# Optimization experiments

Hardware: AMD Instinct MI355X
Metric: run time of the kernel (lower is better)

## Reference

```python
import jax, jax.numpy as jnp
from jax import lax
import numpy as np

S = 1024      # number of superpoints (all valid, 60 pts each >= min_points)
P = 60        # points per superpoint (labels are contiguous blocks)
K = 10        # sample_k FPS representatives
NM = 800      # total number of SAM masks
H = W = 256   # mask image dims
FD = 512      # point feature dim (clip_dim)
SAMPLE_K = 10
RADIUS = 0.2
MASK_THRES = 0.2
SIM_THRES = 0.5
N_MASK = 5
TOP_K = 10


def setup_inputs() -> dict:
    key = jax.random.key(0)
    ks = jax.random.split(key, 8)
    centers = jax.random.normal(ks[0], (S, 3), jnp.float32)
    # tight clusters around centers so the radius-0.2 graph has edges
    pcds = (centers[:, None, :] + 0.03 * jax.random.normal(ks[1], (S, P, 3), jnp.float32)).reshape(S * P, 3)
    spt_labels = jnp.repeat(jnp.arange(S, dtype=jnp.int32), P)
    masks = jax.random.bernoulli(ks[2], 0.05, (NM, H, W))
    y = jax.random.randint(ks[3], (S * P,), 0, H, jnp.int32)
    x = jax.random.randint(ks[4], (S * P,), 0, W, jnp.int32)
    vis = jax.random.bernoulli(ks[5], 0.7, (S * P,)).astype(jnp.int32)
    mapping = jnp.stack([jnp.zeros(S * P, jnp.int32), y, x, vis], axis=1)
    sam_scores = jax.random.uniform(ks[6], (NM,), jnp.float32, 0.5, 1.0)
    point_feas = jax.random.normal(ks[7], (S * P, FD), jnp.float32)
    return {"pcds": pcds, "spt_labels": spt_labels, "masks": masks,
            "mapping": mapping, "sam_scores": sam_scores, "point_feas": point_feas}


def _fps_idx(pts, k):
    # pts: [P,3]. Deterministic start at index 0 (torch version uses a random start).
    d0 = jnp.sum((pts - pts[0]) ** 2, axis=1)
    def step(dist, _):
        idx = jnp.argmax(dist)
        nd = jnp.sum((pts - pts[idx]) ** 2, axis=1)
        return jnp.minimum(dist, nd), idx
    _, rest = lax.scan(step, d0, None, length=k - 1)
    return jnp.concatenate([jnp.zeros((1,), rest.dtype), rest])


def _forward(pcds, sam_scores, point_feas, spt_labels, masks, mapping):
    N = pcds.shape[0]
    pts_g = pcds.reshape(S, P, 3)  # labels are contiguous blocks of size P
    idxs = jax.vmap(lambda p: _fps_idx(lax.stop_gradient(p), SAMPLE_K))(pts_g)      # [S,K]
    reps = jnp.take_along_axis(pts_g, idxs[:, :, None], axis=1)                     # [S,K,3]

    # pairwise min distance between superpoint representative sets
    flat = reps.reshape(S * K, 3)
    sq = jnp.sum(flat ** 2, axis=1)
    d2 = jnp.maximum(sq[:, None] + sq[None, :] - 2.0 * (flat @ flat.T), 0.0)
    d = jnp.sqrt(d2 + 1e-12)
    mind = d.reshape(S, K, S, K).min(axis=(1, 3))                                   # [S,S]
    eye = jnp.eye(S, dtype=bool)
    adj0 = jnp.where((mind < RADIUS) & ~eye, jnp.exp(-mind), 0.0)

    # mask coverage per point, aggregated per superpoint
    vis = mapping[:, 3] == 1
    yy = jnp.clip(mapping[:, 1], 0, H - 1)
    xx = jnp.clip(mapping[:, 2], 0, W - 1)
    coverage = (masks[:, yy, xx].T & vis[:, None]).astype(jnp.float32)              # [N,NM]
    counts = jax.ops.segment_sum(jnp.ones((N,), jnp.float32), spt_labels, num_segments=S)[:, None]
    cov_g = jax.ops.segment_sum(coverage, spt_labels, num_segments=S)               # [S,NM]
    frac = cov_g / (counts + 1e-6)

    # per-mask keep only top_k superpoints by coverage fraction
    _, tki = lax.top_k(frac.T, TOP_K)                                               # [NM,TOP_K]
    tkm = jnp.zeros((NM, S), bool).at[jnp.arange(NM)[:, None], tki].set(True).T      # [S,NM]
    frac = jnp.where(tkm, frac, 0.0)
    contrib = frac >= MASK_THRES                                                     # [S,NM] bool

    # mean point features per superpoint, L2-normalized
    feats = jax.ops.segment_sum(point_feas, spt_labels, num_segments=S) / (counts + 1e-6)
    feats = feats / jnp.maximum(jnp.linalg.norm(feats, axis=1, keepdims=True), 1e-12)

    def row_mod(i):
        mi = contrib[i]                                                              # [NM]
        union = (mi[None, :] | contrib).astype(jnp.float32)                          # [S,NM]
        _, tk = lax.top_k(union, N_MASK)                                             # [S,N_MASK]
        ti = jnp.take_along_axis(jnp.broadcast_to(mi[None, :], (S, NM)), tk, axis=1)
        tj = jnp.take_along_axis(contrib, tk, axis=1)
        inter = (ti & tj).sum(1).astype(jnp.float32)
        uni = (ti | tj).sum(1).astype(jnp.float32)
        ov = inter / (uni + 1e-6)
        sim = jnp.clip((feats @ feats[i] + 1.0) * 0.5, 0.0, 1.0)
        sim = jnp.where(sim < SIM_THRES, 1.0, sim)
        return ov * sim

    mod = lax.map(row_mod, jnp.arange(S))                                            # [S,S], symmetric
    adjacency = jnp.where(adj0 > 0, jnp.maximum(mod, adj0), 0.0)

    weights = frac * sam_scores[None, :]
    conf = jnp.clip(weights.sum(1) / (frac.sum(1) + 1e-6), 0.0, None)
    return adjacency, conf


def reference(pcds, spt_labels, masks, mapping, sam_scores, point_feas):
    return _forward(pcds, sam_scores, point_feas, spt_labels, masks, mapping)
```

## Files before the change

### kernel.cpp

```cpp
#include <hip/hip_runtime.h>
#include <hip/hip_bf16.h>

#define SNUM 1024
#define PNUM 60
#define KFPS 10
#define NMASK 800
#define WORDS 25
#define HWDIM 256
#define FD 512
#define NPTS (SNUM*PNUM)
#define EDGE_CAP (1u<<20)

__device__ __forceinline__ float fmul(float a, float b){ return __fmul_rn(a,b); }
__device__ __forceinline__ float fadd(float a, float b){ return __fadd_rn(a,b); }
__device__ __forceinline__ float fsub(float a, float b){ return __fsub_rn(a,b); }

__device__ __forceinline__ float dist2f(float ax,float ay,float az,float bx,float by,float bz){
    float dx=fsub(ax,bx), dy=fsub(ay,by), dz=fsub(az,bz);
    return fadd(fadd(fmul(dx,dx),fmul(dy,dy)),fmul(dz,dz));
}

__global__ __launch_bounds__(64) void k_initfps(const float* __restrict__ pcds,
                                                float* __restrict__ reps,
                                                unsigned int* __restrict__ zbase,
                                                const unsigned char* __restrict__ m8,
                                                unsigned int* __restrict__ dflag){
    int s = blockIdx.x;
    int l = threadIdx.x;
    if (s < 64){
        int tid = s*64 + l;
        #pragma unroll
        for (int k=0;k<8;++k){
            int wi = tid + k*4096;
            if (wi < 28673) zbase[wi] = 0u;
        }
        #pragma unroll
        for (int k=0;k<16;++k){
            int i = tid*16 + k;
            if ((i & 3) != 0 && m8[i] == 1){ atomicOr(dflag, 1u); break; }
        }
    }
    float x=0.f,y=0.f,z=0.f;
    if (l < PNUM){
        const float* p = pcds + (size_t)(s*PNUM + l)*3;
        x=p[0]; y=p[1]; z=p[2];
    }
    float x0=__shfl(x,0), y0=__shfl(y,0), z0=__shfl(z,0);
    float dist = dist2f(x,y,z,x0,y0,z0);
    int sel[KFPS];
    sel[0]=0;
    #pragma unroll
    for(int it=1; it<KFPS; ++it){
        float v = (l<PNUM)? dist : -INFINITY;
        int idx = l;
        #pragma unroll
        for(int off=32; off; off>>=1){
            float ov = __shfl_xor(v, off);
            int   oi = __shfl_xor(idx, off);
            if (ov > v || (ov==v && oi<idx)){ v=ov; idx=oi; }
        }
        sel[it]=idx;
        float sx=__shfl(x,idx), sy=__shfl(y,idx), sz=__shfl(z,idx);
        float nd = dist2f(x,y,z,sx,sy,sz);
        dist = fminf(dist, nd);
    }
    #pragma unroll
    for(int j=0;j<KFPS;++j){
        float rx=__shfl(x,sel[j]), ry=__shfl(y,sel[j]), rz=__shfl(z,sel[j]);
        if (l==0){
            float* o = reps + (size_t)(s*KFPS+j)*3;
            o[0]=rx; o[1]=ry; o[2]=rz;
        }
    }
}

__global__ __launch_bounds__(256) void k_pack(const unsigned char* __restrict__ m8,
                                              const int* __restrict__ m32,
                                              const unsigned int* __restrict__ flag,
                                              unsigned int* __restrict__ pb){
    __shared__ unsigned int lds[256*WORDS];
    int t = threadIdx.x;
    int wv = t >> 6, lane = t & 63;
    int pixBase = blockIdx.x * 256;
    if (*flag & 1u){
        const unsigned int* base32 = (const unsigned int*)m8;
        int pix4 = (pixBase >> 2) + lane;
        for (int w=wv; w<WORDS; w+=4){
            unsigned int w0=0,w1=0,w2=0,w3=0;
            #pragma unroll
            for (int b=0;b<32;++b){
                unsigned int u = base32[(size_t)(w*32+b)*16384 + pix4];
                w0 |= (u & 1u) << b;
                w1 |= ((u >> 8) & 1u) << b;
                w2 |= ((u >> 16) & 1u) << b;
                w3 |= ((u >> 24) & 1u) << b;
            }
            int p4 = lane*4;
            lds[(p4+0)*WORDS+w]=w0; lds[(p4+1)*WORDS+w]=w1;
            lds[(p4+2)*WORDS+w]=w2; lds[(p4+3)*WORDS+w]=w3;
        }
    } else {
        for (int w=wv; w<WORDS; w+=4){
            for (int i=0;i<4;++i){
                int pixel = pixBase + lane*4 + i;
                unsigned int word = 0;
                #pragma unroll
                for (int b=0;b<32;++b)
                    word |= (unsigned int)(m32[(size_t)(w*32+b)*65536 + pixel] & 1) << b;
                lds[(lane*4+i)*WORDS+w] = word;
            }
        }
    }
    __syncthreads();
    uint4* out4 = (uint4*)(pb + (size_t)pixBase*WORDS);
    const uint4* l4 = (const uint4*)lds;
    for (int u=t; u<1600; u+=256) out4[u] = l4[u];
}

__global__ __launch_bounds__(256) void k_cov(const int* __restrict__ mapping,
                                             const unsigned int* __restrict__ pb,
                                             unsigned char* __restrict__ cntT){
    __shared__ int pxl[8][PNUM];
    int t = threadIdx.x;
    int sBase = blockIdx.x * 8;
    for (int idx=t; idx<8*PNUM; idx+=256){
        int ls = idx / PNUM, p = idx - ls*PNUM;
        const int4 v = ((const int4*)mapping)[(sBase+ls)*PNUM + p];
        int y = min(max(v.y,0),HWDIM-1), x = min(max(v.z,0),HWDIM-1);
        pxl[ls][p] = (v.w==1) ? ((y<<8)|x) : -1;
    }
    __syncthreads();
    int ls = t >> 5, w = t & 31;
    if (w >= WORDS) return;
    unsigned int acc8[8];
    #pragma unroll
    for (int k=0;k<8;++k) acc8[k]=0;
    #pragma unroll 6
    for (int p=0;p<PNUM;++p){
        int px = pxl[ls][p];
        if (px >= 0){
            unsigned int word = pb[(size_t)px*WORDS + w];
            #pragma unroll
            for (int k=0;k<8;++k)
                acc8[k] += (word >> k) & 0x01010101u;
        }
    }
    int s = sBase + ls;
    #pragma unroll
    for (int k=0;k<8;++k)
        #pragma unroll
        for (int j=0;j<4;++j){
            int b = k + 8*j;
            cntT[(size_t)(w*32+b)*SNUM + s] = (unsigned char)((acc8[k] >> (8*j)) & 0xFF);
        }
}

__global__ __launch_bounds__(256) void k_topk(const unsigned char* __restrict__ cntT,
                                              const float* __restrict__ scores,
                                              unsigned int* __restrict__ contrib,
                                              float* __restrict__ wsum,
                                              float* __restrict__ fsum){
    int m = blockIdx.x;
    int t = threadIdx.x;
    __shared__ int hist[64];
    __shared__ int scan_s[256];
    __shared__ int sT, sR;
    if (t < 64) hist[t]=0;
    __syncthreads();
    uchar4 c4 = ((const uchar4*)(cntT + (size_t)m*SNUM))[t];
    int c[4] = {(int)c4.x,(int)c4.y,(int)c4.z,(int)c4.w};
    atomicAdd(&hist[c[0]],1); atomicAdd(&hist[c[1]],1);
    atomicAdd(&hist[c[2]],1); atomicAdd(&hist[c[3]],1);
    __syncthreads();
    if (t==0){
        int running=0, T=0, r=10;
        for(int v=63;v>=0;--v){
            int nr = running + hist[v];
            if (nr >= 10){ T=v; r=10-running; break; }
            running = nr;
        }
        sT=T; sR=r;
    }
    __syncthreads();
    int T=sT, r=sR;
    int eq = (c[0]==T)+(c[1]==T)+(c[2]==T)+(c[3]==T);
    scan_s[t]=eq; __syncthreads();
    for(int off=1;off<256;off<<=1){
        int v = (t>=off)? scan_s[t-off] : 0;
        __syncthreads();
        scan_s[t]+=v;
        __syncthreads();
    }
    int rank = scan_s[t]-eq;
    float sc = scores[m];
    #pragma unroll
    for(int j=0;j<4;++j){
        int s = t*4+j;
        bool selv = (c[j]>T) || (c[j]==T && rank<r);
        if (c[j]==T) rank++;
        if (selv && c[j]>0){
            float frac = (float)c[j]/60.0f;
            atomicAdd(&wsum[s], frac*sc);
            atomicAdd(&fsum[s], frac);
            if (c[j] >= 12)
                atomicOr(&contrib[s*WORDS + (m>>5)], 1u<<(m&31));
        }
    }
}

__global__ __launch_bounds__(256) void k_adj0(const float* __restrict__ reps,
                                              float* __restrict__ out,
                                              unsigned int* __restrict__ ecnt,
                                              unsigned int* __restrict__ edges,
                                              unsigned int* __restrict__ needed,
                                              const float* __restrict__ wsum,
                                              const float* __restrict__ fsum,
                                              float* __restrict__ conf){
    __shared__ float ri[16][KFPS][3], rj[16][KFPS][3];
    __shared__ float sqi[16][KFPS], sqj[16][KFPS];
    int tx = threadIdx.x, ty = threadIdx.y;
    int t = ty*16+tx;
    if (blockIdx.y==0 && blockIdx.x<4){
        int s = blockIdx.x*256 + t;
        conf[s] = fmaxf(wsum[s]/(fsum[s]+1e-6f), 0.0f);
    }
    int i0 = blockIdx.y*16, j0 = blockIdx.x*16;
    for(int u=t; u<16*KFPS*3; u+=256){
        ((float*)ri)[u] = reps[(size_t)i0*KFPS*3 + u];
        ((float*)rj)[u] = reps[(size_t)j0*KFPS*3 + u];
    }
    __syncthreads();
    if (t < 16*KFPS){
        int sp=t/KFPS, k=t%KFPS;
        float x=ri[sp][k][0], y=ri[sp][k][1], z=ri[sp][k][2];
        sqi[sp][k]=fadd(fadd(fmul(x,x),fmul(y,y)),fmul(z,z));
        x=rj[sp][k][0]; y=rj[sp][k][1]; z=rj[sp][k][2];
        sqj[sp][k]=fadd(fadd(fmul(x,x),fmul(y,y)),fmul(z,z));
    }
    __syncthreads();
    int i = i0+ty, j = j0+tx;
    float m2 = INFINITY;
    #pragma unroll 2
    for(int k=0;k<KFPS;++k){
        float ax=ri[ty][k][0], ay=ri[ty][k][1], az=ri[ty][k][2], as=sqi[ty][k];
        #pragma unroll
        for(int l=0;l<KFPS;++l){
            float dot = fadd(fadd(fmul(ax,rj[tx][l][0]),fmul(ay,rj[tx][l][1])),fmul(az,rj[tx][l][2]));
            float d2 = fmaxf(fsub(fadd(as,sqj[tx][l]), fmul(2.0f,dot)), 0.0f);
            m2 = fminf(m2,d2);
        }
    }
    float d = sqrtf(fadd(m2,1e-12f));
    bool edge = (d < 0.2f) && (i!=j);
    out[(size_t)i*SNUM + j] = edge ? expf(-d) : 0.0f;
    if (edge){
        unsigned int e = atomicAdd(ecnt, 1u);
        if (e < EDGE_CAP) edges[e] = ((unsigned int)i<<10) | (unsigned int)j;
        atomicOr(&needed[i], 1u);
        atomicOr(&needed[j], 1u);
    }
}

__global__ __launch_bounds__(256) void k_feats(const float* __restrict__ pf,
                                               const unsigned int* __restrict__ needed,
                                               float* __restrict__ feats){
    int s = blockIdx.x, t = threadIdx.x;
    if (!needed[s]) return;
    int g = t >> 7;
    int c = t & 127;
    const float4* pf4 = (const float4*)pf;
    float4 a = make_float4(0.f,0.f,0.f,0.f);
    for (int p=g; p<PNUM; p+=2){
        float4 v = pf4[(size_t)(s*PNUM+p)*128 + c];
        a.x+=v.x; a.y+=v.y; a.z+=v.z; a.w+=v.w;
    }
    __shared__ float4 part[2][128];
    part[g][c] = a;
    __shared__ float red[256];
    __syncthreads();
    float4 m = make_float4(0.f,0.f,0.f,0.f);
    float ss = 0.f;
    if (g==0){
        float4 b = part[1][c];
        m.x=(a.x+b.x)/60.0f; m.y=(a.y+b.y)/60.0f; m.z=(a.z+b.z)/60.0f; m.w=(a.w+b.w)/60.0f;
        ss = m.x*m.x + m.y*m.y + m.z*m.z + m.w*m.w;
    }
    red[t] = ss; __syncthreads();
    for (int off=128; off; off>>=1){ if (t<off) red[t]+=red[t+off]; __syncthreads(); }
    float denom = fmaxf(sqrtf(red[0]), 1e-12f);
    if (g==0){
        float4 o; o.x=m.x/denom; o.y=m.y/denom; o.z=m.z/denom; o.w=m.w/denom;
        ((float4*)feats)[(size_t)s*128 + c] = o;
    }
}

__global__ __launch_bounds__(64) void k_mod(const unsigned int* __restrict__ ecnt,
                                            const unsigned int* __restrict__ edges,
                                            const unsigned int* __restrict__ contrib,
                                            const float* __restrict__ feats,
                                            float* __restrict__ out){
    unsigned int n = *ecnt; if (n > EDGE_CAP) n = EDGE_CAP;
    int lane = threadIdx.x;
    for (unsigned int e = blockIdx.x; e < n; e += gridDim.x){
        unsigned int pk = edges[e];
        int i = (int)(pk>>10), j = (int)(pk & 1023u);
        const float4* fi = (const float4*)(feats + (size_t)i*FD);
        const float4* fj = (const float4*)(feats + (size_t)j*FD);
        float dot = 0.f;
        #pragma unroll
        for(int r=0;r<2;++r){
            float4 a = fi[lane + 64*r], b = fj[lane + 64*r];
            dot += a.x*b.x + a.y*b.y + a.z*b.z + a.w*b.w;
        }
        #pragma unroll
        for(int off=32;off;off>>=1) dot += __shfl_xor(dot,off);

        unsigned int u=0, aw=0; int cw=0;
        if (lane < WORDS){
            unsigned int bi = contrib[i*WORDS+lane], bj = contrib[j*WORDS+lane];
            u = bi|bj; aw = bi&bj; cw = __popc(u);
        }
        int pre=0, ctot=0;
        for(int k2=0;k2<WORDS;++k2){
            int v=__shfl(cw,k2);
            ctot += v;
            if (k2<lane) pre += v;
        }
        int il=0;
        if (lane<WORDS && pre<5){
            unsigned int x=u;
            int lim = 5-pre;
            #pragma unroll
            for(int q=0;q<5;++q){
                if (q<lim && x){
                    int b = __ffs(x)-1;
                    il += (int)((aw>>b)&1u);
                    x &= x-1;
                }
            }
        }
        #pragma unroll
        for(int off=32;off;off>>=1) il += __shfl_xor(il,off);
        int uni = min(ctot,5);
        float ov = (float)il / ((float)uni + 1e-6f);
        float sim = fminf(fmaxf((dot+1.0f)*0.5f,0.0f),1.0f);
        if (sim < 0.5f) sim = 1.0f;
        float mod = ov*sim;
        if (lane==0){
            size_t o = (size_t)i*SNUM+j;
            out[o] = fmaxf(out[o], mod);
        }
    }
}

extern "C" void kernel_launch(void* const* d_in, const int* in_sizes, int n_in,
                              void* d_out, int out_size, void* d_ws, size_t ws_size,
                              hipStream_t stream){
    const float*         pcds    = (const float*)d_in[0];
    const unsigned char* masks8  = (const unsigned char*)d_in[2];
    const int*           masks32 = (const int*)d_in[2];
    const int*           mapping = (const int*)d_in[3];
    const float*         scores  = (const float*)d_in[4];
    const float*         pf      = (const float*)d_in[5];
    float* out_adj  = (float*)d_out;
    float* out_conf = out_adj + (size_t)SNUM*SNUM;

    char* ws = (char*)d_ws;
    float*         reps    = (float*)(ws + 0);
    unsigned int*  pb      = (unsigned int*)(ws + 131072);
    unsigned char* cntT    = (unsigned char*)(ws + 6684672);
    unsigned int*  contrib = (unsigned int*)(ws + 7503872);
    float*         wsum    = (float*)(ws + 7606272);
    float*         fsum    = (float*)(ws + 7610368);
    unsigned int*  needed  = (unsigned int*)(ws + 7614464);
    unsigned int*  ecnt    = (unsigned int*)(ws + 7618560);
    unsigned int*  dflag   = (unsigned int*)(ws + 7618564);
    unsigned int*  edges   = (unsigned int*)(ws + 7618568);
    float*         feats   = (float*)(ws + 11812880);
    unsigned int*  zbase   = (unsigned int*)(ws + 7503872);

    k_initfps<<<SNUM, 64, 0, stream>>>(pcds, reps, zbase, masks8, dflag);
    k_pack   <<<HWDIM*HWDIM/256, 256, 0, stream>>>(masks8, masks32, dflag, pb);
    k_cov    <<<SNUM/8, 256, 0, stream>>>(mapping, pb, cntT);
    k_topk   <<<NMASK, 256, 0, stream>>>(cntT, scores, contrib, wsum, fsum);
    k_adj0   <<<dim3(64,64), dim3(16,16), 0, stream>>>(reps, out_adj, ecnt, edges, needed, wsum, fsum, out_conf);
    k_feats  <<<SNUM, 256, 0, stream>>>(pf, needed, feats);
    k_mod    <<<1024, 64, 0, stream>>>(ecnt, edges, contrib, feats, out_adj);
}
```

Baseline: 462.6 us.

## Merge independent kernels into combined launches and exploit adjacency symmetry

Folds the coverage counting and the adjacency tile computation into one launch that splits work by block index, and does the same for the top-k mask selection and the per-superpoint feature averaging. The adjacency kernel now computes only upper-triangular 16x16 tiles and writes the transposed tile through shared memory, emitting both edge directions. The top-k prefix scan uses wavefront shuffles instead of a shared-memory barrier loop, and the confidence computation moves into the final kernel. This cuts launch count and roughly halves the distance work. The cost is extra per-block branching, and the triangular tile index is found with a serial loop in each block.

```diff
diff --git a/kernel.cpp b/kernel.cpp
--- a/kernel.cpp
+++ b/kernel.cpp
@@ -10,6 +10,7 @@
 #define FD 512
 #define NPTS (SNUM*PNUM)
 #define EDGE_CAP (1u<<20)
+#define NTILE 2080
 
 __device__ __forceinline__ float fmul(float a, float b){ return __fmul_rn(a,b); }
 __device__ __forceinline__ float fadd(float a, float b){ return __fadd_rn(a,b); }
@@ -117,180 +118,199 @@
     for (int u=t; u<1600; u+=256) out4[u] = l4[u];
 }
 
-__global__ __launch_bounds__(256) void k_cov(const int* __restrict__ mapping,
-                                             const unsigned int* __restrict__ pb,
-                                             unsigned char* __restrict__ cntT){
-    __shared__ int pxl[8][PNUM];
+__global__ __launch_bounds__(256) void k_covadj(const float* __restrict__ reps,
+                                                const int* __restrict__ mapping,
+                                                const unsigned int* __restrict__ pb,
+                                                unsigned char* __restrict__ cntT,
+                                                float* __restrict__ out,
+                                                unsigned int* __restrict__ ecnt,
+                                                unsigned int* __restrict__ edges,
+                                                unsigned int* __restrict__ needed){
+    int bid = blockIdx.x;
     int t = threadIdx.x;
-    int sBase = blockIdx.x * 8;
-    for (int idx=t; idx<8*PNUM; idx+=256){
-        int ls = idx / PNUM, p = idx - ls*PNUM;
-        const int4 v = ((const int4*)mapping)[(sBase+ls)*PNUM + p];
-        int y = min(max(v.y,0),HWDIM-1), x = min(max(v.z,0),HWDIM-1);
-        pxl[ls][p] = (v.w==1) ? ((y<<8)|x) : -1;
-    }
-    __syncthreads();
-    int ls = t >> 5, w = t & 31;
-    if (w >= WORDS) return;
-    unsigned int acc8[8];
-    #pragma unroll
-    for (int k=0;k<8;++k) acc8[k]=0;
-    #pragma unroll 6
-    for (int p=0;p<PNUM;++p){
-        int px = pxl[ls][p];
-        if (px >= 0){
-            unsigned int word = pb[(size_t)px*WORDS + w];
+    if (bid < NTILE){
+        int rem = bid, it = 0;
+        while (rem >= 64 - it){ rem -= 64 - it; ++it; }
+        int jt = it + rem;
+        __shared__ float ri[16][KFPS][3], rj[16][KFPS][3];
+        __shared__ float sqi[16][KFPS], sqj[16][KFPS];
+        __shared__ float tile[16][17];
+        int tx = t & 15, ty = t >> 4;
+        int i0 = it*16, j0 = jt*16;
+        for(int u=t; u<16*KFPS*3; u+=256){
+            ((float*)ri)[u] = reps[(size_t)i0*KFPS*3 + u];
+            ((float*)rj)[u] = reps[(size_t)j0*KFPS*3 + u];
+        }
+        __syncthreads();
+        if (t < 16*KFPS){
+            int sp=t/KFPS, k=t%KFPS;
+            float x=ri[sp][k][0], y=ri[sp][k][1], z=ri[sp][k][2];
+            sqi[sp][k]=fadd(fadd(fmul(x,x),fmul(y,y)),fmul(z,z));
+            x=rj[sp][k][0]; y=rj[sp][k][1]; z=rj[sp][k][2];
+            sqj[sp][k]=fadd(fadd(fmul(x,x),fmul(y,y)),fmul(z,z));
+        }
+        __syncthreads();
+        int i = i0+ty, j = j0+tx;
+        float m2 = INFINITY;
+        #pragma unroll 2
+        for(int k=0;k<KFPS;++k){
+            float ax=ri[ty][k][0], ay=ri[ty][k][1], az=ri[ty][k][2], as=sqi[ty][k];
             #pragma unroll
-            for (int k=0;k<8;++k)
-                acc8[k] += (word >> k) & 0x01010101u;
-        }
-    }
-    int s = sBase + ls;
-    #pragma unroll
-    for (int k=0;k<8;++k)
-        #pragma unroll
-        for (int j=0;j<4;++j){
-            int b = k + 8*j;
-            cntT[(size_t)(w*32+b)*SNUM + s] = (unsigned char)((acc8[k] >> (8*j)) & 0xFF);
-        }
-}
-
-__global__ __launch_bounds__(256) void k_topk(const unsigned char* __restrict__ cntT,
-                                              const float* __restrict__ scores,
-                                              unsigned int* __restrict__ contrib,
-                                              float* __restrict__ wsum,
-                                              float* __restrict__ fsum){
-    int m = blockIdx.x;
+            for(int l=0;l<KFPS;++l){
+                float dot = fadd(fadd(fmul(ax,rj[tx][l][0]),fmul(ay,rj[tx][l][1])),fmul(az,rj[tx][l][2]));
+                float d2 = fmaxf(fsub(fadd(as,sqj[tx][l]), fmul(2.0f,dot)), 0.0f);
+                m2 = fminf(m2,d2);
+            }
+        }
+        float d = sqrtf(fadd(m2,1e-12f));
+        bool edge = (d < 0.2f) && (i!=j);
+        float v = edge ? expf(-d) : 0.0f;
+        out[(size_t)i*SNUM + j] = v;
+        tile[ty][tx] = v;
+        if (edge){
+            if (it != jt){
+                unsigned int e = atomicAdd(ecnt, 2u);
+                if (e+1 < EDGE_CAP){
+                    edges[e]   = ((unsigned int)i<<10) | (unsigned int)j;
+                    edges[e+1] = ((unsigned int)j<<10) | (unsigned int)i;
+                }
+            } else {
+                unsigned int e = atomicAdd(ecnt, 1u);
+                if (e < EDGE_CAP) edges[e] = ((unsigned int)i<<10) | (unsigned int)j;
+            }
+            atomicOr(&needed[i], 1u);
+            atomicOr(&needed[j], 1u);
+        }
+        if (it != jt){
+            __syncthreads();
+            out[(size_t)(j0+ty)*SNUM + i0 + tx] = tile[tx][ty];
+        }
+    } else {
+        __shared__ int pxl[8][PNUM];
+        int sBase = (bid - NTILE) * 8;
+        for (int idx=t; idx<8*PNUM; idx+=256){
+            int ls = idx / PNUM, p = idx - ls*PNUM;
+            const int4 v = ((const int4*)mapping)[(sBase+ls)*PNUM + p];
+            int y = min(max(v.y,0),HWDIM-1), x = min(max(v.z,0),HWDIM-1);
+            pxl[ls][p] = (v.w==1) ? ((y<<8)|x) : -1;
+        }
+        __syncthreads();
+        int ls = t >> 5, w = t & 31;
+        if (w >= WORDS) return;
+        unsigned int acc8[8];
+        #pragma unroll
+        for (int k=0;k<8;++k) acc8[k]=0;
+        #pragma unroll 6
+        for (int p=0;p<PNUM;++p){
+            int px = pxl[ls][p];
+            if (px >= 0){
+                unsigned int word = pb[(size_t)px*WORDS + w];
+                #pragma unroll
+                for (int k=0;k<8;++k)
+                    acc8[k] += (word >> k) & 0x01010101u;
+            }
+        }
+        int s = sBase + ls;
+        #pragma unroll
+        for (int k=0;k<8;++k)
+            #pragma unroll
+            for (int j=0;j<4;++j){
+                int b = k + 8*j;
+                cntT[(size_t)(w*32+b)*SNUM + s] = (unsigned char)((acc8[k] >> (8*j)) & 0xFF);
+            }
+    }
+}
+
+__global__ __launch_bounds__(256) void k_topkfeats(const unsigned char* __restrict__ cntT,
+                                                   const float* __restrict__ scores,
+                                                   unsigned int* __restrict__ contrib,
+                                                   float* __restrict__ wsum,
+                                                   float* __restrict__ fsum,
+                                                   const float* __restrict__ pf,
+                                                   const unsigned int* __restrict__ needed,
+                                                   float* __restrict__ feats){
+    int bid = blockIdx.x;
     int t = threadIdx.x;
-    __shared__ int hist[64];
-    __shared__ int scan_s[256];
-    __shared__ int sT, sR;
-    if (t < 64) hist[t]=0;
-    __syncthreads();
-    uchar4 c4 = ((const uchar4*)(cntT + (size_t)m*SNUM))[t];
-    int c[4] = {(int)c4.x,(int)c4.y,(int)c4.z,(int)c4.w};
-    atomicAdd(&hist[c[0]],1); atomicAdd(&hist[c[1]],1);
-    atomicAdd(&hist[c[2]],1); atomicAdd(&hist[c[3]],1);
-    __syncthreads();
-    if (t==0){
-        int running=0, T=0, r=10;
-        for(int v=63;v>=0;--v){
-            int nr = running + hist[v];
-            if (nr >= 10){ T=v; r=10-running; break; }
-            running = nr;
-        }
-        sT=T; sR=r;
-    }
-    __syncthreads();
-    int T=sT, r=sR;
-    int eq = (c[0]==T)+(c[1]==T)+(c[2]==T)+(c[3]==T);
-    scan_s[t]=eq; __syncthreads();
-    for(int off=1;off<256;off<<=1){
-        int v = (t>=off)? scan_s[t-off] : 0;
-        __syncthreads();
-        scan_s[t]+=v;
-        __syncthreads();
-    }
-    int rank = scan_s[t]-eq;
-    float sc = scores[m];
-    #pragma unroll
-    for(int j=0;j<4;++j){
-        int s = t*4+j;
-        bool selv = (c[j]>T) || (c[j]==T && rank<r);
-        if (c[j]==T) rank++;
-        if (selv && c[j]>0){
-            float frac = (float)c[j]/60.0f;
-            atomicAdd(&wsum[s], frac*sc);
-            atomicAdd(&fsum[s], frac);
-            if (c[j] >= 12)
-                atomicOr(&contrib[s*WORDS + (m>>5)], 1u<<(m&31));
-        }
-    }
-}
-
-__global__ __launch_bounds__(256) void k_adj0(const float* __restrict__ reps,
-                                              float* __restrict__ out,
-                                              unsigned int* __restrict__ ecnt,
-                                              unsigned int* __restrict__ edges,
-                                              unsigned int* __restrict__ needed,
-                                              const float* __restrict__ wsum,
-                                              const float* __restrict__ fsum,
-                                              float* __restrict__ conf){
-    __shared__ float ri[16][KFPS][3], rj[16][KFPS][3];
-    __shared__ float sqi[16][KFPS], sqj[16][KFPS];
-    int tx = threadIdx.x, ty = threadIdx.y;
-    int t = ty*16+tx;
-    if (blockIdx.y==0 && blockIdx.x<4){
-        int s = blockIdx.x*256 + t;
-        conf[s] = fmaxf(wsum[s]/(fsum[s]+1e-6f), 0.0f);
-    }
-    int i0 = blockIdx.y*16, j0 = blockIdx.x*16;
-    for(int u=t; u<16*KFPS*3; u+=256){
-        ((float*)ri)[u] = reps[(size_t)i0*KFPS*3 + u];
-        ((float*)rj)[u] = reps[(size_t)j0*KFPS*3 + u];
-    }
-    __syncthreads();
-    if (t < 16*KFPS){
-        int sp=t/KFPS, k=t%KFPS;
-        float x=ri[sp][k][0], y=ri[sp][k][1], z=ri[sp][k][2];
-        sqi[sp][k]=fadd(fadd(fmul(x,x),fmul(y,y)),fmul(z,z));
-        x=rj[sp][k][0]; y=rj[sp][k][1]; z=rj[sp][k][2];
-        sqj[sp][k]=fadd(fadd(fmul(x,x),fmul(y,y)),fmul(z,z));
-    }
-    __syncthreads();
-    int i = i0+ty, j = j0+tx;
-    float m2 = INFINITY;
-    #pragma unroll 2
-    for(int k=0;k<KFPS;++k){
-        float ax=ri[ty][k][0], ay=ri[ty][k][1], az=ri[ty][k][2], as=sqi[ty][k];
-        #pragma unroll
-        for(int l=0;l<KFPS;++l){
-            float dot = fadd(fadd(fmul(ax,rj[tx][l][0]),fmul(ay,rj[tx][l][1])),fmul(az,rj[tx][l][2]));
-            float d2 = fmaxf(fsub(fadd(as,sqj[tx][l]), fmul(2.0f,dot)), 0.0f);
-            m2 = fminf(m2,d2);
-        }
-    }
-    float d = sqrtf(fadd(m2,1e-12f));
-    bool edge = (d < 0.2f) && (i!=j);
-    out[(size_t)i*SNUM + j] = edge ? expf(-d) : 0.0f;
-    if (edge){
-        unsigned int e = atomicAdd(ecnt, 1u);
-        if (e < EDGE_CAP) edges[e] = ((unsigned int)i<<10) | (unsigned int)j;
-        atomicOr(&needed[i], 1u);
-        atomicOr(&needed[j], 1u);
-    }
-}
-
-__global__ __launch_bounds__(256) void k_feats(const float* __restrict__ pf,
-                                               const unsigned int* __restrict__ needed,
-                                               float* __restrict__ feats){
-    int s = blockIdx.x, t = threadIdx.x;
-    if (!needed[s]) return;
-    int g = t >> 7;
-    int c = t & 127;
-    const float4* pf4 = (const float4*)pf;
-    float4 a = make_float4(0.f,0.f,0.f,0.f);
-    for (int p=g; p<PNUM; p+=2){
-        float4 v = pf4[(size_t)(s*PNUM+p)*128 + c];
-        a.x+=v.x; a.y+=v.y; a.z+=v.z; a.w+=v.w;
-    }
-    __shared__ float4 part[2][128];
-    part[g][c] = a;
-    __shared__ float red[256];
-    __syncthreads();
-    float4 m = make_float4(0.f,0.f,0.f,0.f);
-    float ss = 0.f;
-    if (g==0){
-        float4 b = part[1][c];
-        m.x=(a.x+b.x)/60.0f; m.y=(a.y+b.y)/60.0f; m.z=(a.z+b.z)/60.0f; m.w=(a.w+b.w)/60.0f;
-        ss = m.x*m.x + m.y*m.y + m.z*m.z + m.w*m.w;
-    }
-    red[t] = ss; __syncthreads();
-    for (int off=128; off; off>>=1){ if (t<off) red[t]+=red[t+off]; __syncthreads(); }
-    float denom = fmaxf(sqrtf(red[0]), 1e-12f);
-    if (g==0){
-        float4 o; o.x=m.x/denom; o.y=m.y/denom; o.z=m.z/denom; o.w=m.w/denom;
-        ((float4*)feats)[(size_t)s*128 + c] = o;
+    if (bid < NMASK){
+        int m = bid;
+        __shared__ int hist[64];
+        __shared__ int wsums[4];
+        __shared__ int sT, sR;
+        if (t < 64) hist[t]=0;
+        __syncthreads();
+        uchar4 c4 = ((const uchar4*)(cntT + (size_t)m*SNUM))[t];
+        int c[4] = {(int)c4.x,(int)c4.y,(int)c4.z,(int)c4.w};
+        atomicAdd(&hist[c[0]],1); atomicAdd(&hist[c[1]],1);
+        atomicAdd(&hist[c[2]],1); atomicAdd(&hist[c[3]],1);
+        __syncthreads();
+        if (t==0){
+            int running=0, T=0, r=10;
+            for(int v=63;v>=0;--v){
+                int nr = running + hist[v];
+                if (nr >= 10){ T=v; r=10-running; break; }
+                running = nr;
+            }
+            sT=T; sR=r;
+        }
+        __syncthreads();
+        int T=sT, r=sR;
+        int eq = (c[0]==T)+(c[1]==T)+(c[2]==T)+(c[3]==T);
+        int incl = eq;
+        #pragma unroll
+        for (int off=1; off<64; off<<=1){
+            int v = __shfl_up(incl, off);
+            if ((t & 63) >= off) incl += v;
+        }
+        if ((t & 63) == 63) wsums[t>>6] = incl;
+        __syncthreads();
+        int base = 0;
+        #pragma unroll
+        for (int wv=0; wv<4; ++wv)
+            if (wv < (t>>6)) base += wsums[wv];
+        int rank = base + incl - eq;
+        float sc = scores[m];
+        #pragma unroll
+        for(int j=0;j<4;++j){
+            int s = t*4+j;
+            bool selv = (c[j]>T) || (c[j]==T && rank<r);
+            if (c[j]==T) rank++;
+            if (selv && c[j]>0){
+                float frac = (float)c[j]/60.0f;
+                atomicAdd(&wsum[s], frac*sc);
+                atomicAdd(&fsum[s], frac);
+                if (c[j] >= 12)
+                    atomicOr(&contrib[s*WORDS + (m>>5)], 1u<<(m&31));
+            }
+        }
+    } else {
+        int s = bid - NMASK;
+        if (!needed[s]) return;
+        int g = t >> 7;
+        int c = t & 127;
+        const float4* pf4 = (const float4*)pf;
+        float4 a = make_float4(0.f,0.f,0.f,0.f);
+        for (int p=g; p<PNUM; p+=2){
+            float4 v = pf4[(size_t)(s*PNUM+p)*128 + c];
+            a.x+=v.x; a.y+=v.y; a.z+=v.z; a.w+=v.w;
+        }
+        __shared__ float4 part[2][128];
+        part[g][c] = a;
+        __shared__ float red[256];
+        __syncthreads();
+        float4 m = make_float4(0.f,0.f,0.f,0.f);
+        float ss = 0.f;
+        if (g==0){
+            float4 b = part[1][c];
+            m.x=(a.x+b.x)/60.0f; m.y=(a.y+b.y)/60.0f; m.z=(a.z+b.z)/60.0f; m.w=(a.w+b.w)/60.0f;
+            ss = m.x*m.x + m.y*m.y + m.z*m.z + m.w*m.w;
+        }
+        red[t] = ss; __syncthreads();
+        for (int off=128; off; off>>=1){ if (t<off) red[t]+=red[t+off]; __syncthreads(); }
+        float denom = fmaxf(sqrtf(red[0]), 1e-12f);
+        if (g==0){
+            float4 o; o.x=m.x/denom; o.y=m.y/denom; o.z=m.z/denom; o.w=m.w/denom;
+            ((float4*)feats)[(size_t)s*128 + c] = o;
+        }
     }
 }
 
@@ -298,9 +318,16 @@
                                             const unsigned int* __restrict__ edges,
                                             const unsigned int* __restrict__ contrib,
                                             const float* __restrict__ feats,
+                                            const float* __restrict__ wsum,
+                                            const float* __restrict__ fsum,
+                                            float* __restrict__ conf,
                                             float* __restrict__ out){
+    int lane = threadIdx.x;
+    if (blockIdx.x < 16){
+        int s = blockIdx.x*64 + lane;
+        conf[s] = fmaxf(wsum[s]/(fsum[s]+1e-6f), 0.0f);
+    }
     unsigned int n = *ecnt; if (n > EDGE_CAP) n = EDGE_CAP;
-    int lane = threadIdx.x;
     for (unsigned int e = blockIdx.x; e < n; e += gridDim.x){
         unsigned int pk = edges[e];
         int i = (int)(pk>>10), j = (int)(pk & 1023u);
@@ -379,11 +406,9 @@
     float*         feats   = (float*)(ws + 11812880);
     unsigned int*  zbase   = (unsigned int*)(ws + 7503872);
 
-    k_initfps<<<SNUM, 64, 0, stream>>>(pcds, reps, zbase, masks8, dflag);
-    k_pack   <<<HWDIM*HWDIM/256, 256, 0, stream>>>(masks8, masks32, dflag, pb);
-    k_cov    <<<SNUM/8, 256, 0, stream>>>(mapping, pb, cntT);
-    k_topk   <<<NMASK, 256, 0, stream>>>(cntT, scores, contrib, wsum, fsum);
-    k_adj0   <<<dim3(64,64), dim3(16,16), 0, stream>>>(reps, out_adj, ecnt, edges, needed, wsum, fsum, out_conf);
-    k_feats  <<<SNUM, 256, 0, stream>>>(pf, needed, feats);
-    k_mod    <<<1024, 64, 0, stream>>>(ecnt, edges, contrib, feats, out_adj);
-}
+    k_initfps  <<<SNUM, 64, 0, stream>>>(pcds, reps, zbase, masks8, dflag);
+    k_pack     <<<HWDIM*HWDIM/256, 256, 0, stream>>>(masks8, masks32, dflag, pb);
+    k_covadj   <<<NTILE + SNUM/8, 256, 0, stream>>>(reps, mapping, pb, cntT, out_adj, ecnt, edges, needed);
+    k_topkfeats<<<NMASK + SNUM, 256, 0, stream>>>(cntT, scores, contrib, wsum, fsum, pf, needed, feats);
+    k_mod      <<<1024, 64, 0, stream>>>(ecnt, edges, contrib, feats, wsum, fsum, out_conf, out_adj);
+}
```

New measurement: 432.0 us. 6.6% less time.
